# Performance work log

Measured on AMD Instinct MI355X. Metric: run time of the kernel, lower is better.

Reference implementation:

```python
import jax, jax.numpy as jnp
import numpy as np

N_NODES = 6000
DEG = 16
N_EDGES = N_NODES * DEG
D_MODEL = 256
D_MSG = 64
D_FF = 4 * D_MODEL
N_LAYERS = 3
N_SPECIES = 108
RBF_BINS = D_MODEL
RBF_VMIN, RBF_VMAX = 0.0, 8.0


def setup_inputs():
    key = jax.random.key(0)
    ks = jax.random.split(key, 16)
    rng = np.random.default_rng(0)
    # graph: each node i has DEG in-edges (dst block-structured), random sources
    atomic_number = jnp.asarray(rng.integers(1, N_SPECIES, N_NODES), dtype=jnp.int32)
    dst = np.repeat(np.arange(N_NODES), DEG)
    src = rng.integers(0, N_NODES, N_EDGES)
    # angle graph t: nodes = edges of g; edges = all ordered pairs of in-edges sharing dst
    pq = np.array([(p, q) for p in range(DEG) for q in range(DEG) if p != q], dtype=np.int64)
    off = (np.arange(N_NODES) * DEG)[:, None]
    t_src = (off + pq[:, 0][None, :]).reshape(-1)
    t_dst = (off + pq[:, 1][None, :]).reshape(-1)
    r = jax.random.normal(ks[0], (N_EDGES, 3), dtype=jnp.float32) * 2.0  # bond vectors, |r|~3A
    s_dm = 1.0 / np.sqrt(D_MODEL)
    s_dmsg = 1.0 / np.sqrt(D_MSG)
    s_ff = 1.0 / np.sqrt(D_FF)
    return {
        'r': r,
        'atomic_number': atomic_number,
        'src': jnp.asarray(src, dtype=jnp.int32),
        'dst': jnp.asarray(dst, dtype=jnp.int32),
        't_src': jnp.asarray(t_src, dtype=jnp.int32),
        't_dst': jnp.asarray(t_dst, dtype=jnp.int32),
        'emb': jax.random.normal(ks[1], (N_SPECIES, D_MODEL), dtype=jnp.float32),
        'Wsrc': jax.random.normal(ks[2], (N_LAYERS, D_MSG, D_MODEL), dtype=jnp.float32) * s_dm,
        'bsrc': jnp.zeros((N_LAYERS, D_MSG), jnp.float32),
        'Wdst': jax.random.normal(ks[3], (N_LAYERS, D_MSG, D_MODEL), dtype=jnp.float32) * s_dm,
        'bdst': jnp.zeros((N_LAYERS, D_MSG), jnp.float32),
        'Wedge': jax.random.normal(ks[4], (N_LAYERS, D_MSG, D_MODEL), dtype=jnp.float32) * s_dm,
        'bedge': jnp.zeros((N_LAYERS, D_MSG), jnp.float32),
        'attn': jax.random.normal(ks[5], (N_LAYERS, D_MSG), dtype=jnp.float32) * s_dmsg,
        'W1': jax.random.normal(ks[6], (N_LAYERS, D_FF, D_MSG), dtype=jnp.float32) * s_dmsg,
        'b1': jnp.zeros((N_LAYERS, D_FF), jnp.float32),
        'W2': jax.random.normal(ks[7], (N_LAYERS, D_MODEL, D_FF), dtype=jnp.float32) * s_ff,
        'b2': jnp.zeros((N_LAYERS, D_MODEL), jnp.float32),
        'Wfc': jax.random.normal(ks[8], (1, D_MODEL), dtype=jnp.float32) * s_dm,
        'bfc': jnp.zeros((1,), jnp.float32),
    }


def _segment_softmax(logits, seg, num):
    m = jax.ops.segment_max(logits, seg, num_segments=num)
    ex = jnp.exp(logits - m[seg])
    z = jax.ops.segment_sum(ex, seg, num_segments=num)
    return ex / z[seg]


def reference(r, atomic_number, src, dst, t_src, t_dst, emb, Wsrc, bsrc, Wdst, bdst,
              Wedge, bedge, attn, W1, b1, W2, b2, Wfc, bfc):
    x = emb[atomic_number]                                   # [N, d_model]
    d = jnp.linalg.norm(r, axis=1)                           # [E]
    centers = jnp.linspace(RBF_VMIN, RBF_VMAX, RBF_BINS, dtype=r.dtype)
    gamma = 1.0 / (centers[1] - centers[0])
    y = jnp.exp(-gamma * (d[:, None] - centers[None, :]) ** 2)  # [E, d_model]
    rhat = r / d[:, None]
    # cos angle between edge pairs (sign of -r cancels in u_dot_v)
    cos_jik = jnp.clip(jnp.sum(rhat[t_src] * rhat[t_dst], axis=1), -1.0 + 1e-6, 1.0 - 1e-6)
    nch = jnp.arange(D_MSG, dtype=r.dtype)
    z_jik = jnp.cos(nch[None, :] * jnp.arccos(cos_jik)[:, None])  # Chebyshev T_k(cos) [T, 64]
    for l in range(N_LAYERS):
        xj = x @ Wsrc[l].T + bsrc[l]                          # [N, 64]
        xi = x @ Wdst[l].T + bdst[l]
        xij = xj[src] + xi[dst] + (y @ Wedge[l].T + bedge[l])  # [E, 64]
        e_jik = jax.nn.silu(z_jik + xij[t_src] + xij[t_dst])   # [T, 64]
        logits = e_jik @ attn[l]                               # [T]
        a = _segment_softmax(logits, t_dst, N_EDGES)           # edge_softmax over angle graph
        ft = jax.ops.segment_sum(a[:, None] * xij[t_src], t_dst, num_segments=N_EDGES)  # [E, 64]
        xn = jax.ops.segment_sum(ft, dst, num_segments=N_NODES)  # scatter to nodes [N, 64]
        x = jax.nn.silu(xn @ W1[l].T + b1[l]) @ W2[l].T + b2[l]  # FFN -> [N, d_model]
    atomwise = x @ Wfc.T + bfc                                  # [N, 1]
    return jnp.squeeze(jnp.mean(atomwise, axis=0))              # AvgPooling (eV/atom)


if __name__ == '__main__':
    out = reference(**setup_inputs())
    print(out)
```

## Files before the change

### kernel.cpp

```cpp
#include <hip/hip_runtime.h>

#define N_NODES 6000
#define DEG_    16
#define N_EDGES (N_NODES*DEG_)
#define D_MODEL 256
#define D_MSG   64
#define D_FF    1024

typedef __bf16 bf16x8 __attribute__((ext_vector_type(8)));
typedef float floatx4 __attribute__((ext_vector_type(4)));

__device__ __forceinline__ float silu_f(float v) {
    return v * __builtin_amdgcn_rcpf(1.0f + __expf(-v));
}
__device__ __forceinline__ float b2f(unsigned short u) {
    union { unsigned int i; float f; } v; v.i = ((unsigned int)u) << 16; return v.f;
}
__device__ __forceinline__ unsigned short f2b(float f) {
    union { float f; unsigned int i; } v; v.f = f;
    unsigned int r = (v.i + 0x7FFFu + ((v.i >> 16) & 1u)) >> 16;
    return (unsigned short)r;
}

#define WSRC_OFF 0
#define WDST_OFF 49152
#define WCVT_TOTAL 98304
#define CVT4_BLOCKS (WCVT_TOTAL/4/256)
#define EMB4_BLOCKS (N_NODES*D_MODEL/4/256)
#define GEOM_BLOCKS (N_EDGES/256)
#define WPACKE_BLOCKS 24
#define WPACK1_BLOCKS 96
__global__ __launch_bounds__(256) void prep_kernel(
    const float* __restrict__ Wsrc, const float* __restrict__ Wdst,
    const float* __restrict__ Wedge, const float* __restrict__ W1,
    unsigned short* __restrict__ wbf_out,
    const int* __restrict__ an, const float* __restrict__ emb,
    unsigned short* __restrict__ x,
    const float* __restrict__ r, float* __restrict__ d, float* __restrict__ rhat,
    unsigned short* __restrict__ wedgep,
    unsigned short* __restrict__ w1p) {
    int b = blockIdx.x;
    int t = threadIdx.x;
    if (b < CVT4_BLOCKS) {
        int i = (b*256 + t) * 4;
        const float* sp = (i < WDST_OFF) ? (Wsrc + i) : (Wdst + (i - WDST_OFF));
        float4 v = *(const float4*)sp;
        *(ushort4*)(wbf_out + i) = make_ushort4(f2b(v.x), f2b(v.y), f2b(v.z), f2b(v.w));
    } else if (b < CVT4_BLOCKS + EMB4_BLOCKS) {
        int i4 = (b - CVT4_BLOCKS)*256 + t;
        int node = i4 >> 6, c4 = i4 & 63;
        float4 v = *(const float4*)(emb + (size_t)an[node]*D_MODEL + c4*4);
        *(ushort4*)(x + (size_t)node*D_MODEL + c4*4) =
            make_ushort4(f2b(v.x), f2b(v.y), f2b(v.z), f2b(v.w));
    } else if (b < CVT4_BLOCKS + EMB4_BLOCKS + GEOM_BLOCKS) {
        int e = (b - CVT4_BLOCKS - EMB4_BLOCKS)*256 + t;
        float xx = r[e*3+0], yy = r[e*3+1], zz = r[e*3+2];
        float n = sqrtf(xx*xx + yy*yy + zz*zz);
        d[e] = n;
        float inv = 1.0f / n;
        *(float4*)(rhat + (size_t)e*4) = make_float4(xx*inv, yy*inv, zz*inv, 0.f);
    } else if (b < CVT4_BLOCKS + EMB4_BLOCKS + GEOM_BLOCKS + WPACKE_BLOCKS) {
        int wb = b - (CVT4_BLOCKS + EMB4_BLOCKS + GEOM_BLOCKS);
        int i = wb*256 + t;
        int lane = i & 63, ks = (i >> 6) & 7, rem = i >> 9;
        int ns = rem % 3, w = rem / 3;
        int row = 48*w + ns*16 + (lane & 15);
        int col = ks*32 + (lane >> 4)*8;
        const float* sp = Wedge + (size_t)row*256 + col;
        float4 v0 = *(const float4*)sp;
        float4 v1 = *(const float4*)(sp + 4);
        unsigned short h[8] = { f2b(v0.x), f2b(v0.y), f2b(v0.z), f2b(v0.w),
                                f2b(v1.x), f2b(v1.y), f2b(v1.z), f2b(v1.w) };
        *(uint4*)(wedgep + (size_t)i*8) = *(uint4*)h;
    } else {
        int wb = b - (CVT4_BLOCKS + EMB4_BLOCKS + GEOM_BLOCKS + WPACKE_BLOCKS);
        int i2 = wb*256 + t;
        int lp = i2 >> 13;
        int e = i2 & 8191;
        int lane = e & 63, j = (e >> 6) & 1, wv = (e >> 7) & 3, f = e >> 9;
        int row = f*64 + wv*16 + (lane & 15);
        int col = j*32 + (lane >> 4)*8;
        const float* sp = W1 + (size_t)lp*65536 + (size_t)row*64 + col;
        float4 v0 = *(const float4*)sp;
        float4 v1 = *(const float4*)(sp + 4);
        unsigned short h[8] = { f2b(v0.x), f2b(v0.y), f2b(v0.z), f2b(v0.w),
                                f2b(v1.x), f2b(v1.y), f2b(v1.z), f2b(v1.w) };
        *(uint4*)(w1p + (size_t)i2*8) = *(uint4*)h;
    }
}

__global__ __launch_bounds__(256) void wcomb_kernel(
    const float* __restrict__ Wsrc, const float* __restrict__ bsrc,
    const float* __restrict__ Wdst, const float* __restrict__ bdst,
    const float* __restrict__ W2, const float* __restrict__ b2,
    const float* __restrict__ Wfc, const float* __restrict__ bfc,
    unsigned short* __restrict__ wcomb,
    float* __restrict__ bcomb,
    float* __restrict__ wfc2,
    float* __restrict__ out) {
    int b = blockIdx.x;
    int t = threadIdx.x;
    if (b < 64) {
        int lp  = 1 + (b >> 5);
        int wb2 = b & 31;
        const float* W2f = W2 + (size_t)(lp-1)*262144;
        const float* wm[4];
        #pragma unroll
        for (int i = 0; i < 4; ++i) {
            int row = wb2*4 + i;
            wm[i] = (row < 64) ? (Wsrc + (size_t)lp*16384 + row*256)
                               : (Wdst + (size_t)lp*16384 + (row-64)*256);
        }
        float acc[4][4] = {};
        int c0 = t*4;
        #pragma unroll 8
        for (int c = 0; c < 256; ++c) {
            float4 w2v = *(const float4*)(W2f + (size_t)c*1024 + c0);
            #pragma unroll
            for (int i = 0; i < 4; ++i) {
                float w = wm[i][c];
                acc[i][0] = fmaf(w, w2v.x, acc[i][0]);
                acc[i][1] = fmaf(w, w2v.y, acc[i][1]);
                acc[i][2] = fmaf(w, w2v.z, acc[i][2]);
                acc[i][3] = fmaf(w, w2v.w, acc[i][3]);
            }
        }
        int fc = t >> 4, j = (t >> 3) & 1, lq = (t >> 1) & 3, cpos = (t & 1) * 4;
        #pragma unroll
        for (int i = 0; i < 4; ++i) {
            int row = wb2*4 + i;
            int wv = row >> 5, ns = (row >> 4) & 1, lr = row & 15;
            *(ushort4*)(wcomb + (size_t)(lp-1)*131072
                        + (size_t)fc*8192 + wv*2048 + ns*1024 + j*512 + (lq*16+lr)*8 + cpos) =
                make_ushort4(f2b(acc[i][0]), f2b(acc[i][1]), f2b(acc[i][2]), f2b(acc[i][3]));
        }
    } else if (b < 68) {
        int c = (b - 64)*256 + t;
        const float* W2f = W2 + 2*262144;
        float a0 = 0.f, a1 = 0.f, a2 = 0.f, a3 = 0.f;
        #pragma unroll 4
        for (int k = 0; k < 256; k += 4) {
            a0 = fmaf(Wfc[k+0], W2f[(size_t)(k+0)*1024 + c], a0);
            a1 = fmaf(Wfc[k+1], W2f[(size_t)(k+1)*1024 + c], a1);
            a2 = fmaf(Wfc[k+2], W2f[(size_t)(k+2)*1024 + c], a2);
            a3 = fmaf(Wfc[k+3], W2f[(size_t)(k+3)*1024 + c], a3);
        }
        wfc2[c] = (a0 + a1) + (a2 + a3);
    } else {
        int lp = 1 + (t >> 7);
        int row = t & 127;
        const float* b2l = b2 + (lp-1)*256;
        const float* wmrow = (row < 64) ? (Wsrc + (size_t)lp*16384 + row*256)
                                        : (Wdst + (size_t)lp*16384 + (row-64)*256);
        float acc = 0.f;
        #pragma unroll 8
        for (int c = 0; c < 256; ++c) acc += wmrow[c] * b2l[c];
        acc += (row < 64) ? bsrc[lp*64 + row] : bdst[lp*64 + (row-64)];
        bcomb[(lp-1)*128 + row] = acc;
        if (t == 0) {
            float bo = 0.f;
            const float* b23 = b2 + 2*256;
            #pragma unroll 8
            for (int c = 0; c < 256; ++c) bo += Wfc[c] * b23[c];
            out[0] = bo + bfc[0];
        }
    }
}

#define EPITCH 264
#define APITCH 40
#define MCP 72
__global__ __launch_bounds__(256) void eplg_kernel(
    const unsigned short* __restrict__ Bwp,
    const float* __restrict__ bias,
    const float* __restrict__ dvec,
    unsigned short* __restrict__ C,
    const unsigned short* __restrict__ A,
    const unsigned short* __restrict__ B1g,
    const unsigned short* __restrict__ B2g,
    const float* __restrict__ bias1,
    const float* __restrict__ bias2,
    unsigned short* __restrict__ Cg) {
    __shared__ __align__(16) unsigned short sm[64*EPITCH];
    const int t = threadIdx.x;
    const int w = t >> 6, lane = t & 63, lr = lane & 15, lq = lane >> 4;

    if (blockIdx.x < 1500) {
        unsigned short* As = sm;
        const int m0 = blockIdx.x * 64;
        const int arow = t >> 2, achk = t & 3;

        float dv = dvec[m0 + arow];
        const float gamma = 31.875f;
        const float step  = 8.0f / 255.0f;
        #pragma unroll
        for (int c32 = 0; c32 < 8; ++c32) {
            int kb = c32*32 + achk*8;
            unsigned short h[8];
            #pragma unroll
            for (int j = 0; j < 8; ++j) {
                float tt = dv - (float)(kb+j)*step;
                h[j] = f2b(__expf(-gamma*tt*tt));
            }
            *(uint4*)(&As[arow*EPITCH + kb]) = *(uint4*)h;
        }
        __syncthreads();

        const unsigned short* Bp = Bwp + (size_t)w*12288 + lane*8;

        floatx4 acc[4][3] = {};
        uint4 pb[3];
        #pragma unroll
        for (int ns = 0; ns < 3; ++ns)
            pb[ns] = *(const uint4*)(Bp + ns*4096);

        for (int k0 = 0; k0 < 256; k0 += 32) {
            int ks = k0 >> 5;
            uint4 cb[3];
            cb[0] = pb[0]; cb[1] = pb[1]; cb[2] = pb[2];
            if (k0 + 32 < 256) {
                #pragma unroll
                for (int ns = 0; ns < 3; ++ns)
                    pb[ns] = *(const uint4*)(Bp + ns*4096 + (ks+1)*512);
            }
            bf16x8 af[4];
            #pragma unroll
            for (int mi = 0; mi < 4; ++mi)
                af[mi] = *(const bf16x8*)(&As[(mi*16 + lr)*EPITCH + k0 + lq*8]);
            #pragma unroll
            for (int mi = 0; mi < 4; ++mi) {
                #pragma unroll
                for (int ns = 0; ns < 3; ++ns)
                    acc[mi][ns] = __builtin_amdgcn_mfma_f32_16x16x32_bf16(
                        af[mi], *(const bf16x8*)&cb[ns], acc[mi][ns], 0, 0, 0);
            }
        }

        #pragma unroll
        for (int ns = 0; ns < 3; ++ns) {
            int bc = 48*w + ns*16 + lr;
            float bv = bias[bc];
            #pragma unroll
            for (int mi = 0; mi < 4; ++mi) {
                #pragma unroll
                for (int rg = 0; rg < 4; ++rg) {
                    int row = m0 + mi*16 + lq*4 + rg;
                    C[(size_t)row*192 + bc] = f2b(acc[mi][ns][rg] + bv);
                }
            }
        }
        return;
    }
    {
        unsigned short* As = sm;
        unsigned short* Bs = sm + 2560;
        unsigned short* Cs = sm;
        const int bid2 = blockIdx.x - 1500;
        const int bx = bid2 & 1;
        const int m0 = (bid2 >> 1) * 64;
        const unsigned short* B = bx ? B2g : B1g;
        const float* biasl = bx ? bias2 : bias1;
        const int n0 = bx * 64;
        const int K = 256, M = N_NODES, lda = 256, ldb = 256, ldc = 128;

        const int arow = t >> 2, achk = t & 3;

        floatx4 acc[4] = {};
        uint4 pa, pb;
        {
            int gm = m0 + arow;
            pa = (gm < M) ? *(const uint4*)(A + (size_t)gm*lda + achk*8) : make_uint4(0,0,0,0);
        }
        pb = *(const uint4*)(B + (size_t)arow*ldb + achk*8);

        for (int k0 = 0; k0 < K; k0 += 32) {
            *(uint4*)(&As[arow*APITCH + achk*8]) = pa;
            *(uint4*)(&Bs[arow*APITCH + achk*8]) = pb;
            __syncthreads();
            if (k0 + 32 < K) {
                int kn = k0 + 32;
                int gm = m0 + arow;
                pa = (gm < M) ? *(const uint4*)(A + (size_t)gm*lda + kn + achk*8) : make_uint4(0,0,0,0);
                pb = *(const uint4*)(B + (size_t)arow*ldb + kn + achk*8);
            }
            bf16x8 af, bfr[4];
            af = *(const bf16x8*)(&As[(w*16 + lr)*APITCH + lq*8]);
            #pragma unroll
            for (int ns = 0; ns < 4; ++ns)
                bfr[ns] = *(const bf16x8*)(&Bs[(ns*16 + lr)*APITCH + lq*8]);
            #pragma unroll
            for (int ns = 0; ns < 4; ++ns)
                acc[ns] = __builtin_amdgcn_mfma_f32_16x16x32_bf16(af, bfr[ns], acc[ns], 0,0,0);
            __syncthreads();
        }
        #pragma unroll
        for (int ns = 0; ns < 4; ++ns) {
            int bc = ns*16 + lr;
            float bv = biasl[bc];
            #pragma unroll
            for (int rg = 0; rg < 4; ++rg) {
                int lrow = w*16 + lq*4 + rg;
                Cs[lrow*MCP + bc] = f2b(acc[ns][rg] + bv);
            }
        }
        __syncthreads();
        #pragma unroll
        for (int it = 0; it < 2; ++it) {
            int i = t + it*256;
            int row = i >> 3, c8 = i & 7;
            int gm = m0 + row;
            if (gm < M)
                *(uint4*)(Cg + (size_t)gm*ldc + n0 + c8*8) = *(const uint4*)(Cs + row*MCP + c8*8);
        }
    }
}

#define HP 72
#define CP2 136
__global__ __launch_bounds__(256) void ffw_kernel(
    const unsigned short* __restrict__ XN,
    const unsigned short* __restrict__ W1p,
    const float* __restrict__ b1l,
    const unsigned short* __restrict__ WCp,
    const float* __restrict__ bcl,
    unsigned short* __restrict__ XO,
    int M) {
    __shared__ __align__(16) unsigned short s_h[16*HP];
    __shared__ __align__(16) unsigned short s_c[16*CP2];
    const int t = threadIdx.x;
    const int wv = t >> 6, lane = t & 63, lr = lane & 15, lq = lane >> 4;
    const int m0 = blockIdx.x * 16;

    int ga = m0 + lr;
    bool aok = ga < M;
    uint4 a0 = aok ? *(const uint4*)(XN + (size_t)ga*64 + lq*8) : make_uint4(0,0,0,0);
    uint4 a1 = aok ? *(const uint4*)(XN + (size_t)ga*64 + 32 + lq*8) : make_uint4(0,0,0,0);

    floatx4 acc2[2] = {};

    const unsigned short* W1b = W1p + (size_t)wv*1024 + lane*8;
    const unsigned short* WCb = WCp + (size_t)wv*2048 + lane*8;

    uint4 pb1[2], pb2[4];
    pb1[0] = *(const uint4*)(W1b);
    pb1[1] = *(const uint4*)(W1b + 512);
    pb2[0] = *(const uint4*)(WCb);
    pb2[1] = *(const uint4*)(WCb + 512);
    pb2[2] = *(const uint4*)(WCb + 1024);
    pb2[3] = *(const uint4*)(WCb + 1536);

    for (int f = 0; f < 16; ++f) {
        uint4 cb1_0 = pb1[0], cb1_1 = pb1[1];
        uint4 cb2_0 = pb2[0], cb2_1 = pb2[1], cb2_2 = pb2[2], cb2_3 = pb2[3];
        float bv1 = b1l[f*64 + wv*16 + lr];
        if (f < 15) {
            const unsigned short* n1 = W1b + (f+1)*4096;
            const unsigned short* n2 = WCb + (f+1)*8192;
            pb1[0] = *(const uint4*)(n1);
            pb1[1] = *(const uint4*)(n1 + 512);
            pb2[0] = *(const uint4*)(n2);
            pb2[1] = *(const uint4*)(n2 + 512);
            pb2[2] = *(const uint4*)(n2 + 1024);
            pb2[3] = *(const uint4*)(n2 + 1536);
        }
        floatx4 hacc = {};
        hacc = __builtin_amdgcn_mfma_f32_16x16x32_bf16(
            *(const bf16x8*)&a0, *(const bf16x8*)&cb1_0, hacc, 0,0,0);
        hacc = __builtin_amdgcn_mfma_f32_16x16x32_bf16(
            *(const bf16x8*)&a1, *(const bf16x8*)&cb1_1, hacc, 0,0,0);
        {
            int col = wv*16 + lr;
            #pragma unroll
            for (int rg = 0; rg < 4; ++rg) {
                int row = lq*4 + rg;
                s_h[row*HP + col] = f2b(silu_f(hacc[rg] + bv1));
            }
        }
        __syncthreads();
        bf16x8 ha0 = *(const bf16x8*)(&s_h[lr*HP + lq*8]);
        bf16x8 ha1 = *(const bf16x8*)(&s_h[lr*HP + 32 + lq*8]);
        acc2[0] = __builtin_amdgcn_mfma_f32_16x16x32_bf16(ha0, *(const bf16x8*)&cb2_0, acc2[0], 0,0,0);
        acc2[0] = __builtin_amdgcn_mfma_f32_16x16x32_bf16(ha1, *(const bf16x8*)&cb2_1, acc2[0], 0,0,0);
        acc2[1] = __builtin_amdgcn_mfma_f32_16x16x32_bf16(ha0, *(const bf16x8*)&cb2_2, acc2[1], 0,0,0);
        acc2[1] = __builtin_amdgcn_mfma_f32_16x16x32_bf16(ha1, *(const bf16x8*)&cb2_3, acc2[1], 0,0,0);
        __syncthreads();
    }

    #pragma unroll
    for (int ns = 0; ns < 2; ++ns) {
        int col = wv*32 + ns*16 + lr;
        float bv = bcl[col];
        #pragma unroll
        for (int rg = 0; rg < 4; ++rg) {
            int row = lq*4 + rg;
            s_c[row*CP2 + col] = f2b(acc2[ns][rg] + bv);
        }
    }
    __syncthreads();
    {
        int row = t >> 4, c8 = t & 15;
        int gm = m0 + row;
        if (gm < M)
            *(uint4*)(XO + (size_t)gm*128 + c8*8) = *(const uint4*)(s_c + row*CP2 + c8*8);
    }
}

__global__ __launch_bounds__(256) void ffa_kernel(
    const unsigned short* __restrict__ XN,
    const unsigned short* __restrict__ W1p,
    const float* __restrict__ b1l,
    const float* __restrict__ wfc2,
    float* __restrict__ out, int M) {
    __shared__ float red[256];
    const int t = threadIdx.x;
    const int wv = t >> 6, lane = t & 63, lr = lane & 15, lq = lane >> 4;
    const int m0 = blockIdx.x * 16;

    int ga = m0 + lr;
    bool aok = ga < M;
    uint4 a0 = aok ? *(const uint4*)(XN + (size_t)ga*64 + lq*8) : make_uint4(0,0,0,0);
    uint4 a1 = aok ? *(const uint4*)(XN + (size_t)ga*64 + 32 + lq*8) : make_uint4(0,0,0,0);

    const unsigned short* W1b = W1p + (size_t)wv*1024 + lane*8;
    uint4 pb0 = *(const uint4*)(W1b);
    uint4 pb1 = *(const uint4*)(W1b + 512);

    float partial = 0.f;
    for (int f = 0; f < 16; ++f) {
        uint4 c0 = pb0, c1 = pb1;
        if (f < 15) {
            pb0 = *(const uint4*)(W1b + (f+1)*4096);
            pb1 = *(const uint4*)(W1b + (f+1)*4096 + 512);
        }
        floatx4 hacc = {};
        hacc = __builtin_amdgcn_mfma_f32_16x16x32_bf16(
            *(const bf16x8*)&a0, *(const bf16x8*)&c0, hacc, 0,0,0);
        hacc = __builtin_amdgcn_mfma_f32_16x16x32_bf16(
            *(const bf16x8*)&a1, *(const bf16x8*)&c1, hacc, 0,0,0);
        float bv1 = b1l[f*64 + wv*16 + lr];
        float wvv = wfc2[f*64 + wv*16 + lr];
        #pragma unroll
        for (int rg = 0; rg < 4; ++rg) {
            int gm = m0 + lq*4 + rg;
            if (gm < M) partial += silu_f(hacc[rg] + bv1) * wvv;
        }
    }
    red[t] = partial;
    __syncthreads();
    for (int off = 128; off > 0; off >>= 1) {
        if (t < off) red[t] += red[t+off];
        __syncthreads();
    }
    if (t == 0) atomicAdd(out, red[0] * (1.0f/(float)N_NODES));
}

__global__ __launch_bounds__(256) void angle_kernel(
    const unsigned short* __restrict__ xjxi,
    const unsigned short* __restrict__ eproj,
    const float* __restrict__ rhat,
    const int*   __restrict__ src,
    const float* __restrict__ attn,
    unsigned short* __restrict__ xn) {
    __shared__ __align__(16) float s_xij[16][68];
    __shared__ float s_rhat[16][4];
    __shared__ float s_logit[16][17];
    __shared__ float s_e[16][17];
    __shared__ float s_m[16], s_zi[16];
    __shared__ float s_w[16];
    const int tt = threadIdx.x;
    const int node = blockIdx.x;

    if (tt < 16) {
        float4 rv = *(const float4*)(rhat + (size_t)(node*DEG_ + tt)*4);
        s_rhat[tt][0] = rv.x; s_rhat[tt][1] = rv.y; s_rhat[tt][2] = rv.z; s_rhat[tt][3] = 0.f;
        s_e[tt][tt] = 0.f;
    }
    {
        int p = tt >> 4, c4 = tt & 15;
        int e = node*DEG_ + p;
        int se = src[e];
        ushort4 aj = *(const ushort4*)(xjxi + (size_t)se*128 + c4*4);
        ushort4 ai = *(const ushort4*)(xjxi + (size_t)node*128 + 64 + c4*4);
        ushort4 ae = *(const ushort4*)(eproj + (size_t)e*192 + c4*4);
        s_xij[p][c4*4+0] = b2f(aj.x) + b2f(ai.x) + b2f(ae.x);
        s_xij[p][c4*4+1] = b2f(aj.y) + b2f(ai.y) + b2f(ae.y);
        s_xij[p][c4*4+2] = b2f(aj.z) + b2f(ai.z) + b2f(ae.z);
        s_xij[p][c4*4+3] = b2f(aj.w) + b2f(ai.w) + b2f(ae.w);
    }
    __syncthreads();
    int pp = 0, qq = 0;
    float lg = 0.f;
    if (tt < 240) {
        int pair = tt >> 1, half = tt & 1;
        pp = (int)((1.0f + sqrtf(8.0f*(float)pair + 1.0f)) * 0.5f);
        qq = pair - ((pp*(pp-1)) >> 1);
        float c = s_rhat[pp][0]*s_rhat[qq][0] + s_rhat[pp][1]*s_rhat[qq][1]
                + s_rhat[pp][2]*s_rhat[qq][2];
        c = fminf(fmaxf(c, -0.999999f), 0.999999f);
        float c2 = 2.0f * c;
        float tk0, tk1;
        if (half) {
            float T2  = fmaf(c2, c, -1.0f);
            float T3  = fmaf(2.0f*T2,  c,   -c);
            float T4  = fmaf(2.0f*T2,  T2,  -1.0f);
            float T7  = fmaf(2.0f*T4,  T3,  -c);
            float T8  = fmaf(2.0f*T4,  T4,  -1.0f);
            float T15 = fmaf(2.0f*T8,  T7,  -c);
            float T16 = fmaf(2.0f*T8,  T8,  -1.0f);
            float T31 = fmaf(2.0f*T16, T15, -c);
            float T32 = fmaf(2.0f*T16, T16, -1.0f);
            float T33 = fmaf(2.0f*T32, c,   -T31);
            tk0 = T32; tk1 = T33;
        } else {
            tk0 = 1.0f; tk1 = c;
        }
        const float* xp = &s_xij[pp][0] + half*32;
        const float* xq = &s_xij[qq][0] + half*32;
        const float* at = attn + half*32;
        float acc = 0.f;
        #pragma unroll
        for (int k0 = 0; k0 < 32; k0 += 4) {
            float4 xp4 = *(const float4*)(xp + k0);
            float4 xq4 = *(const float4*)(xq + k0);
            float a0 = at[k0+0], a1 = at[k0+1], a2 = at[k0+2], a3 = at[k0+3];
            float v0 = tk0 + xp4.x + xq4.x;
            acc = fmaf(a0, silu_f(v0), acc);
            { float tn2 = c2*tk1 - tk0; tk0 = tk1; tk1 = tn2; }
            float v1 = tk0 + xp4.y + xq4.y;
            acc = fmaf(a1, silu_f(v1), acc);
            { float tn2 = c2*tk1 - tk0; tk0 = tk1; tk1 = tn2; }
            float v2 = tk0 + xp4.z + xq4.z;
            acc = fmaf(a2, silu_f(v2), acc);
            { float tn2 = c2*tk1 - tk0; tk0 = tk1; tk1 = tn2; }
            float v3 = tk0 + xp4.w + xq4.w;
            acc = fmaf(a3, silu_f(v3), acc);
            { float tn2 = c2*tk1 - tk0; tk0 = tk1; tk1 = tn2; }
        }
        lg = acc;
    }
    lg += __shfl_xor(lg, 1);
    if (tt < 240 && (tt & 1) == 0) {
        s_logit[pp][qq] = lg;
        s_logit[qq][pp] = lg;
    }
    __syncthreads();
    if (tt < 16) {
        int q = tt;
        float mx = -1e30f;
        #pragma unroll
        for (int p = 0; p < 16; ++p) if (p != q) mx = fmaxf(mx, s_logit[p][q]);
        s_m[q] = mx;
    }
    __syncthreads();
    if (tt < 120) {
        int p2 = (int)((1.0f + sqrtf(8.0f*(float)tt + 1.0f)) * 0.5f);
        int q2 = tt - ((p2*(p2-1)) >> 1);
        float l = s_logit[p2][q2];
        s_e[p2][q2] = __expf(l - s_m[q2]);
        s_e[q2][p2] = __expf(l - s_m[p2]);
    }
    __syncthreads();
    if (tt < 16) {
        int q = tt;
        float z = 0.f;
        #pragma unroll
        for (int p = 0; p < 16; ++p) z += s_e[p][q];
        s_zi[q] = __builtin_amdgcn_rcpf(z);
    }
    __syncthreads();
    if (tt < 16) {
        int p = tt;
        float sw = 0.f;
        #pragma unroll
        for (int q = 0; q < 16; ++q) sw += s_e[p][q] * s_zi[q];
        s_w[p] = sw;
    }
    __syncthreads();
    if (tt < 64) {
        float acc = 0.f;
        #pragma unroll
        for (int p = 0; p < 16; ++p) acc += s_w[p] * s_xij[p][tt];
        xn[(size_t)node*64 + tt] = f2b(acc);
    }
}

extern "C" void kernel_launch(void* const* d_in, const int* in_sizes, int n_in,
                              void* d_out, int out_size, void* d_ws, size_t ws_size,
                              hipStream_t stream) {
    (void)in_sizes; (void)n_in; (void)out_size; (void)ws_size;
    const float* r    = (const float*)d_in[0];
    const int*   an   = (const int*)  d_in[1];
    const int*   src  = (const int*)  d_in[2];
    const float* emb  = (const float*)d_in[6];
    const float* Wsrc = (const float*)d_in[7];
    const float* bsrc = (const float*)d_in[8];
    const float* Wdst = (const float*)d_in[9];
    const float* bdst = (const float*)d_in[10];
    const float* Wedge= (const float*)d_in[11];
    const float* bedge= (const float*)d_in[12];
    const float* attn = (const float*)d_in[13];
    const float* W1   = (const float*)d_in[14];
    const float* b1   = (const float*)d_in[15];
    const float* W2   = (const float*)d_in[16];
    const float* b2   = (const float*)d_in[17];
    const float* Wfc  = (const float*)d_in[18];
    const float* bfc  = (const float*)d_in[19];

    char* ws = (char*)d_ws;
    float* d_d              = (float*)(ws);
    float* d_rhat           = (float*)(ws + 384000);
    unsigned short* wbf     = (unsigned short*)(ws + 1920000);
    unsigned short* d_x     = (unsigned short*)(ws + 4180992);
    unsigned short* d_xjxi  = (unsigned short*)(ws + 7252992);
    unsigned short* d_eproj = (unsigned short*)(ws + 8788992);
    unsigned short* d_xn    = (unsigned short*)(ws + 45652992);
    unsigned short* d_wcomb = (unsigned short*)(ws + 46420992);
    float* d_bcomb          = (float*)(ws + 46945280);
    float* d_wfc2           = (float*)(ws + 46946304);
    unsigned short* d_wedgep= (unsigned short*)(ws + 46950400);
    unsigned short* d_w1p   = (unsigned short*)(ws + 47048704);
    float* out = (float*)d_out;

    unsigned short* wsrc_bf  = wbf + WSRC_OFF;
    unsigned short* wdst_bf  = wbf + WDST_OFF;

    prep_kernel<<<CVT4_BLOCKS + EMB4_BLOCKS + GEOM_BLOCKS + WPACKE_BLOCKS + WPACK1_BLOCKS,
                  256, 0, stream>>>(
        Wsrc, Wdst, Wedge, W1, wbf, an, emb, d_x, r, d_d, d_rhat, d_wedgep, d_w1p);

    eplg_kernel<<<1500 + 188, 256, 0, stream>>>(
        d_wedgep, bedge, d_d, d_eproj,
        d_x, wsrc_bf, wdst_bf, bsrc, bdst, d_xjxi);

    wcomb_kernel<<<69, 256, 0, stream>>>(
        Wsrc, bsrc, Wdst, bdst, W2, b2, Wfc, bfc,
        d_wcomb, d_bcomb, d_wfc2, out);

    angle_kernel<<<N_NODES, 256, 0, stream>>>(
        d_xjxi, d_eproj, d_rhat, src, attn, d_xn);
    ffw_kernel<<<375, 256, 0, stream>>>(
        d_xn, d_w1p, b1, d_wcomb, d_bcomb, d_xjxi, N_NODES);

    angle_kernel<<<N_NODES, 256, 0, stream>>>(
        d_xjxi, d_eproj + 64, d_rhat, src, attn + 64, d_xn);
    ffw_kernel<<<375, 256, 0, stream>>>(
        d_xn, d_w1p + 65536, b1 + 1024, d_wcomb + 131072, d_bcomb + 128, d_xjxi, N_NODES);

    angle_kernel<<<N_NODES, 256, 0, stream>>>(
        d_xjxi, d_eproj + 128, d_rhat, src, attn + 128, d_xn);
    ffa_kernel<<<375, 256, 0, stream>>>(
        d_xn, d_w1p + 131072, b1 + 2048, d_wfc2, out, N_NODES);
}
```

Measured before the change: 239.6 us.

## Fold weight-combine kernel into eplg launch and parallelize angle softmax with shuffles

Removes the separate wcomb_kernel launch and runs its 69 blocks as extra blocks of eplg_kernel, which drops one launch and lets the weight-combine work overlap the edge projection. In angle_kernel, the serial 16-thread softmax max/exp/sum/weight passes are replaced by a 256-thread layout. Each thread handles one (p,q) pair and reduces with wave shuffles, cutting barriers from four to two. The diagonal is masked by setting its logit to -1e30. The fused kernel carries more parameters and mixes block roles, which may raise register use.

```diff
diff --git a/kernel.cpp b/kernel.cpp
--- a/kernel.cpp
+++ b/kernel.cpp
@@ -89,84 +89,6 @@
     }
 }
 
-__global__ __launch_bounds__(256) void wcomb_kernel(
-    const float* __restrict__ Wsrc, const float* __restrict__ bsrc,
-    const float* __restrict__ Wdst, const float* __restrict__ bdst,
-    const float* __restrict__ W2, const float* __restrict__ b2,
-    const float* __restrict__ Wfc, const float* __restrict__ bfc,
-    unsigned short* __restrict__ wcomb,
-    float* __restrict__ bcomb,
-    float* __restrict__ wfc2,
-    float* __restrict__ out) {
-    int b = blockIdx.x;
-    int t = threadIdx.x;
-    if (b < 64) {
-        int lp  = 1 + (b >> 5);
-        int wb2 = b & 31;
-        const float* W2f = W2 + (size_t)(lp-1)*262144;
-        const float* wm[4];
-        #pragma unroll
-        for (int i = 0; i < 4; ++i) {
-            int row = wb2*4 + i;
-            wm[i] = (row < 64) ? (Wsrc + (size_t)lp*16384 + row*256)
-                               : (Wdst + (size_t)lp*16384 + (row-64)*256);
-        }
-        float acc[4][4] = {};
-        int c0 = t*4;
-        #pragma unroll 8
-        for (int c = 0; c < 256; ++c) {
-            float4 w2v = *(const float4*)(W2f + (size_t)c*1024 + c0);
-            #pragma unroll
-            for (int i = 0; i < 4; ++i) {
-                float w = wm[i][c];
-                acc[i][0] = fmaf(w, w2v.x, acc[i][0]);
-                acc[i][1] = fmaf(w, w2v.y, acc[i][1]);
-                acc[i][2] = fmaf(w, w2v.z, acc[i][2]);
-                acc[i][3] = fmaf(w, w2v.w, acc[i][3]);
-            }
-        }
-        int fc = t >> 4, j = (t >> 3) & 1, lq = (t >> 1) & 3, cpos = (t & 1) * 4;
-        #pragma unroll
-        for (int i = 0; i < 4; ++i) {
-            int row = wb2*4 + i;
-            int wv = row >> 5, ns = (row >> 4) & 1, lr = row & 15;
-            *(ushort4*)(wcomb + (size_t)(lp-1)*131072
-                        + (size_t)fc*8192 + wv*2048 + ns*1024 + j*512 + (lq*16+lr)*8 + cpos) =
-                make_ushort4(f2b(acc[i][0]), f2b(acc[i][1]), f2b(acc[i][2]), f2b(acc[i][3]));
-        }
-    } else if (b < 68) {
-        int c = (b - 64)*256 + t;
-        const float* W2f = W2 + 2*262144;
-        float a0 = 0.f, a1 = 0.f, a2 = 0.f, a3 = 0.f;
-        #pragma unroll 4
-        for (int k = 0; k < 256; k += 4) {
-            a0 = fmaf(Wfc[k+0], W2f[(size_t)(k+0)*1024 + c], a0);
-            a1 = fmaf(Wfc[k+1], W2f[(size_t)(k+1)*1024 + c], a1);
-            a2 = fmaf(Wfc[k+2], W2f[(size_t)(k+2)*1024 + c], a2);
-            a3 = fmaf(Wfc[k+3], W2f[(size_t)(k+3)*1024 + c], a3);
-        }
-        wfc2[c] = (a0 + a1) + (a2 + a3);
-    } else {
-        int lp = 1 + (t >> 7);
-        int row = t & 127;
-        const float* b2l = b2 + (lp-1)*256;
-        const float* wmrow = (row < 64) ? (Wsrc + (size_t)lp*16384 + row*256)
-                                        : (Wdst + (size_t)lp*16384 + (row-64)*256);
-        float acc = 0.f;
-        #pragma unroll 8
-        for (int c = 0; c < 256; ++c) acc += wmrow[c] * b2l[c];
-        acc += (row < 64) ? bsrc[lp*64 + row] : bdst[lp*64 + (row-64)];
-        bcomb[(lp-1)*128 + row] = acc;
-        if (t == 0) {
-            float bo = 0.f;
-            const float* b23 = b2 + 2*256;
-            #pragma unroll 8
-            for (int c = 0; c < 256; ++c) bo += Wfc[c] * b23[c];
-            out[0] = bo + bfc[0];
-        }
-    }
-}
-
 #define EPITCH 264
 #define APITCH 40
 #define MCP 72
@@ -180,7 +102,14 @@
     const unsigned short* __restrict__ B2g,
     const float* __restrict__ bias1,
     const float* __restrict__ bias2,
-    unsigned short* __restrict__ Cg) {
+    unsigned short* __restrict__ Cg,
+    const float* __restrict__ Wsrc, const float* __restrict__ Wdst,
+    const float* __restrict__ W2, const float* __restrict__ b2,
+    const float* __restrict__ Wfc, const float* __restrict__ bfc,
+    unsigned short* __restrict__ wcomb,
+    float* __restrict__ bcomb,
+    float* __restrict__ wfc2,
+    float* __restrict__ out) {
     __shared__ __align__(16) unsigned short sm[64*EPITCH];
     const int t = threadIdx.x;
     const int w = t >> 6, lane = t & 63, lr = lane & 15, lq = lane >> 4;
@@ -251,7 +180,7 @@
         }
         return;
     }
-    {
+    if (blockIdx.x < 1688) {
         unsigned short* As = sm;
         unsigned short* Bs = sm + 2560;
         unsigned short* Cs = sm;
@@ -311,6 +240,75 @@
             int gm = m0 + row;
             if (gm < M)
                 *(uint4*)(Cg + (size_t)gm*ldc + n0 + c8*8) = *(const uint4*)(Cs + row*MCP + c8*8);
+        }
+        return;
+    }
+    {
+        int b = blockIdx.x - 1688;
+        if (b < 64) {
+            int lp  = 1 + (b >> 5);
+            int wb2 = b & 31;
+            const float* W2f = W2 + (size_t)(lp-1)*262144;
+            const float* wm[4];
+            #pragma unroll
+            for (int i = 0; i < 4; ++i) {
+                int row = wb2*4 + i;
+                wm[i] = (row < 64) ? (Wsrc + (size_t)lp*16384 + row*256)
+                                   : (Wdst + (size_t)lp*16384 + (row-64)*256);
+            }
+            float acc[4][4] = {};
+            int c0 = t*4;
+            #pragma unroll 8
+            for (int c = 0; c < 256; ++c) {
+                float4 w2v = *(const float4*)(W2f + (size_t)c*1024 + c0);
+                #pragma unroll
+                for (int i = 0; i < 4; ++i) {
+                    float wv2 = wm[i][c];
+                    acc[i][0] = fmaf(wv2, w2v.x, acc[i][0]);
+                    acc[i][1] = fmaf(wv2, w2v.y, acc[i][1]);
+                    acc[i][2] = fmaf(wv2, w2v.z, acc[i][2]);
+                    acc[i][3] = fmaf(wv2, w2v.w, acc[i][3]);
+                }
+            }
+            int fc = t >> 4, j = (t >> 3) & 1, lq2 = (t >> 1) & 3, cpos = (t & 1) * 4;
+            #pragma unroll
+            for (int i = 0; i < 4; ++i) {
+                int row = wb2*4 + i;
+                int wv2 = row >> 5, ns = (row >> 4) & 1, lr2 = row & 15;
+                *(ushort4*)(wcomb + (size_t)(lp-1)*131072
+                            + (size_t)fc*8192 + wv2*2048 + ns*1024 + j*512 + (lq2*16+lr2)*8 + cpos) =
+                    make_ushort4(f2b(acc[i][0]), f2b(acc[i][1]), f2b(acc[i][2]), f2b(acc[i][3]));
+            }
+        } else if (b < 68) {
+            int c = (b - 64)*256 + t;
+            const float* W2f = W2 + 2*262144;
+            float a0 = 0.f, a1 = 0.f, a2 = 0.f, a3 = 0.f;
+            #pragma unroll 4
+            for (int k = 0; k < 256; k += 4) {
+                a0 = fmaf(Wfc[k+0], W2f[(size_t)(k+0)*1024 + c], a0);
+                a1 = fmaf(Wfc[k+1], W2f[(size_t)(k+1)*1024 + c], a1);
+                a2 = fmaf(Wfc[k+2], W2f[(size_t)(k+2)*1024 + c], a2);
+                a3 = fmaf(Wfc[k+3], W2f[(size_t)(k+3)*1024 + c], a3);
+            }
+            wfc2[c] = (a0 + a1) + (a2 + a3);
+        } else {
+            int lp = 1 + (t >> 7);
+            int row = t & 127;
+            const float* b2l = b2 + (lp-1)*256;
+            const float* wmrow = (row < 64) ? (Wsrc + (size_t)lp*16384 + row*256)
+                                            : (Wdst + (size_t)lp*16384 + (row-64)*256);
+            float acc = 0.f;
+            #pragma unroll 8
+            for (int c = 0; c < 256; ++c) acc += wmrow[c] * b2l[c];
+            acc += (row < 64) ? bias1[lp*64 + row] : bias2[lp*64 + (row-64)];
+            bcomb[(lp-1)*128 + row] = acc;
+            if (t == 0) {
+                float bo = 0.f;
+                const float* b23 = b2 + 2*256;
+                #pragma unroll 8
+                for (int c = 0; c < 256; ++c) bo += Wfc[c] * b23[c];
+                out[0] = bo + bfc[0];
+            }
         }
     }
 }
@@ -464,8 +462,7 @@
     __shared__ __align__(16) float s_xij[16][68];
     __shared__ float s_rhat[16][4];
     __shared__ float s_logit[16][17];
-    __shared__ float s_e[16][17];
-    __shared__ float s_m[16], s_zi[16];
+    __shared__ float s_a[16][17];
     __shared__ float s_w[16];
     const int tt = threadIdx.x;
     const int node = blockIdx.x;
@@ -473,7 +470,7 @@
     if (tt < 16) {
         float4 rv = *(const float4*)(rhat + (size_t)(node*DEG_ + tt)*4);
         s_rhat[tt][0] = rv.x; s_rhat[tt][1] = rv.y; s_rhat[tt][2] = rv.z; s_rhat[tt][3] = 0.f;
-        s_e[tt][tt] = 0.f;
+        s_logit[tt][tt] = -1e30f;
     }
     {
         int p = tt >> 4, c4 = tt & 15;
@@ -544,36 +541,31 @@
         s_logit[qq][pp] = lg;
     }
     __syncthreads();
-    if (tt < 16) {
-        int q = tt;
-        float mx = -1e30f;
-        #pragma unroll
-        for (int p = 0; p < 16; ++p) if (p != q) mx = fmaxf(mx, s_logit[p][q]);
-        s_m[q] = mx;
+    {
+        int q = tt >> 4, p = tt & 15;
+        float l = s_logit[p][q];
+        float m = l;
+        m = fmaxf(m, __shfl_xor(m, 1));
+        m = fmaxf(m, __shfl_xor(m, 2));
+        m = fmaxf(m, __shfl_xor(m, 4));
+        m = fmaxf(m, __shfl_xor(m, 8));
+        float e = __expf(l - m);
+        float z = e;
+        z += __shfl_xor(z, 1);
+        z += __shfl_xor(z, 2);
+        z += __shfl_xor(z, 4);
+        z += __shfl_xor(z, 8);
+        s_a[p][q] = e * __builtin_amdgcn_rcpf(z);
     }
     __syncthreads();
-    if (tt < 120) {
-        int p2 = (int)((1.0f + sqrtf(8.0f*(float)tt + 1.0f)) * 0.5f);
-        int q2 = tt - ((p2*(p2-1)) >> 1);
-        float l = s_logit[p2][q2];
-        s_e[p2][q2] = __expf(l - s_m[q2]);
-        s_e[q2][p2] = __expf(l - s_m[p2]);
-    }
-    __syncthreads();
-    if (tt < 16) {
-        int q = tt;
-        float z = 0.f;
-        #pragma unroll
-        for (int p = 0; p < 16; ++p) z += s_e[p][q];
-        s_zi[q] = __builtin_amdgcn_rcpf(z);
-    }
-    __syncthreads();
-    if (tt < 16) {
-        int p = tt;
-        float sw = 0.f;
-        #pragma unroll
-        for (int q = 0; q < 16; ++q) sw += s_e[p][q] * s_zi[q];
-        s_w[p] = sw;
+    {
+        int p = tt >> 4, q = tt & 15;
+        float a = s_a[p][q];
+        a += __shfl_xor(a, 1);
+        a += __shfl_xor(a, 2);
+        a += __shfl_xor(a, 4);
+        a += __shfl_xor(a, 8);
+        if (q == 0) s_w[p] = a;
     }
     __syncthreads();
     if (tt < 64) {
@@ -628,12 +620,10 @@
                   256, 0, stream>>>(
         Wsrc, Wdst, Wedge, W1, wbf, an, emb, d_x, r, d_d, d_rhat, d_wedgep, d_w1p);
 
-    eplg_kernel<<<1500 + 188, 256, 0, stream>>>(
+    eplg_kernel<<<1500 + 188 + 69, 256, 0, stream>>>(
         d_wedgep, bedge, d_d, d_eproj,
-        d_x, wsrc_bf, wdst_bf, bsrc, bdst, d_xjxi);
-
-    wcomb_kernel<<<69, 256, 0, stream>>>(
-        Wsrc, bsrc, Wdst, bdst, W2, b2, Wfc, bfc,
+        d_x, wsrc_bf, wdst_bf, bsrc, bdst, d_xjxi,
+        Wsrc, Wdst, W2, b2, Wfc, bfc,
         d_wcomb, d_bcomb, d_wfc2, out);
 
     angle_kernel<<<N_NODES, 256, 0, stream>>>(
```

New measurement: 229.4 us. 4.3% less time.
